# Kernel tuning notes

Hardware: AMD Instinct MI355X
Metric: run time of the kernel (lower is better)

Reference implementation:

```python
import jax, jax.numpy as jnp
import numpy as np

EMBED = 1024
HEADS = 16
HEAD_DIM = EMBED // HEADS


def setup_inputs() -> dict:
    key = jax.random.key(0)
    ks = jax.random.split(key, 8)
    N, S = 4, 2048
    values = jax.random.normal(ks[0], (N, S, EMBED), dtype=jnp.float32)
    keys = jax.random.normal(ks[1], (N, S, EMBED), dtype=jnp.float32)
    query = jax.random.normal(ks[2], (N, S, EMBED), dtype=jnp.float32)
    mask = jnp.ones((N, 1, 1, S), dtype=jnp.int32)
    sd = 1.0 / np.sqrt(HEAD_DIM)
    Wv = jax.random.uniform(ks[3], (HEAD_DIM, HEAD_DIM), jnp.float32, -sd, sd)
    Wk = jax.random.uniform(ks[4], (HEAD_DIM, HEAD_DIM), jnp.float32, -sd, sd)
    Wq = jax.random.uniform(ks[5], (HEAD_DIM, HEAD_DIM), jnp.float32, -sd, sd)
    so = 1.0 / np.sqrt(EMBED)
    Wo = jax.random.uniform(ks[6], (EMBED, EMBED), jnp.float32, -so, so)
    bo = jax.random.uniform(ks[7], (EMBED,), jnp.float32, -so, so)
    return {"values": values, "keys": keys, "query": query, "mask": mask,
            "Wv": Wv, "Wk": Wk, "Wq": Wq, "Wo": Wo, "bo": bo}


def reference(values, keys, query, mask, Wv, Wk, Wq, Wo, bo):
    N, Sq, _ = query.shape
    # split heads: (N, L, H, D)
    v = values.reshape(N, -1, HEADS, HEAD_DIM)
    k = keys.reshape(N, -1, HEADS, HEAD_DIM)
    q = query.reshape(N, Sq, HEADS, HEAD_DIM)
    # per-head linear projections (torch Linear: x @ W.T)
    v = jnp.einsum('nlhd,ed->nlhe', v, Wv)
    k = jnp.einsum('nlhd,ed->nlhe', k, Wk)
    q = jnp.einsum('nqhd,ed->nqhe', q, Wq)
    # energy: (N, H, Q, K)
    energy = jnp.einsum('nqhd,nkhd->nhqk', q, k)
    energy = jnp.where(mask == 0, jnp.float32(-1e20), energy)
    # NOTE: original scales by sqrt(embed_size), not sqrt(head_dim)
    attention = jax.nn.softmax(energy / jnp.sqrt(jnp.float32(EMBED)), axis=3)
    out = jnp.einsum('nhql,nlhd->nqhd', attention, v).reshape(N, Sq, EMBED)
    return out @ Wo.T + bo
```

## Files before the change

### kernel.cpp

```cpp
#include <hip/hip_runtime.h>
#include <hip/hip_bf16.h>

typedef __bf16 bf16x8 __attribute__((ext_vector_type(8)));
typedef __bf16 bf16x4 __attribute__((ext_vector_type(4)));
typedef __bf16 bf16x2 __attribute__((ext_vector_type(2)));
typedef float  f32x4  __attribute__((ext_vector_type(4)));
typedef float  f32x16 __attribute__((ext_vector_type(16)));
typedef unsigned int u32;
typedef u32 u32x2 __attribute__((ext_vector_type(2)));
typedef u32 u32x4 __attribute__((ext_vector_type(4)));

#define S_  2048
#define E_  1024
#define NH_ 64

__device__ __forceinline__ f32x4 mfma16(bf16x8 a, bf16x8 b, f32x4 c) {
    return __builtin_amdgcn_mfma_f32_16x16x32_bf16(a, b, c, 0, 0, 0);
}
__device__ __forceinline__ f32x16 mfma32(bf16x8 a, bf16x8 b, f32x16 c) {
    return __builtin_amdgcn_mfma_f32_32x32x16_bf16(a, b, c, 0, 0, 0);
}
__device__ __forceinline__ u32 pack2(float a, float b) {
    bf16x2 t; t[0] = (__bf16)a; t[1] = (__bf16)b;
    return __builtin_bit_cast(u32, t);
}
__device__ __forceinline__ void swap32(u32& a, u32& b) {
    asm("v_permlane32_swap_b32 %0, %1" : "+v"(a), "+v"(b));
}
__device__ __forceinline__ f32x16 zero16() {
    f32x16 z;
#pragma unroll
    for (int i = 0; i < 16; ++i) z[i] = 0.f;
    return z;
}
__device__ __forceinline__ void gload_lds16(const void* g, void* l) {
    __builtin_amdgcn_global_load_lds(
        (const __attribute__((address_space(1))) unsigned int*)g,
        (__attribute__((address_space(3))) unsigned int*)l, 16, 0, 0);
}

__global__ __launch_bounds__(256) void k_cast_wo(const float* __restrict__ Wo,
                                                 __bf16* __restrict__ Wob) {
    int i = (blockIdx.x * 256 + threadIdx.x) * 8;
    int o = i >> 10, e0 = i & 1023;
    float4 a = *(const float4*)(Wo + i);
    float4 b = *(const float4*)(Wo + i + 4);
    bf16x8 f;
    f[0] = (__bf16)a.x; f[1] = (__bf16)a.y; f[2] = (__bf16)a.z; f[3] = (__bf16)a.w;
    f[4] = (__bf16)b.x; f[5] = (__bf16)b.y; f[6] = (__bf16)b.z; f[7] = (__bf16)b.w;
    int e_swz = (e0 & ~63) | ((e0 & 63) ^ ((o & 7) << 3));
    *(bf16x8*)(Wob + (size_t)o * 1024 + e_swz) = f;
}

#define TP 72
__global__ __launch_bounds__(256) void k_proj(const float* __restrict__ vin,
                                              const float* __restrict__ kin,
                                              const float* __restrict__ qin,
                                              const float* __restrict__ Wv,
                                              const float* __restrict__ Wk,
                                              const float* __restrict__ Wq,
                                              __bf16* __restrict__ Qws,
                                              __bf16* __restrict__ Kws,
                                              __bf16* __restrict__ Vt) {
    __shared__ __align__(16) __bf16 tile[64 * TP];
    const int z = blockIdx.z;
    const float* in = (z == 0) ? vin : ((z == 1) ? kin : qin);
    const float* W  = (z == 0) ? Wv  : ((z == 1) ? Wk  : Wq);
    const float scale = (z == 2) ? 0.04508422f : 1.0f;
    const int bid  = blockIdx.x;
    const int nh   = bid >> 3;
    const int sbase = (bid & 7) << 8;
    const int n = nh >> 4, h = nh & 15;
    const int lane = threadIdx.x & 63, wid = threadIdx.x >> 6;
    const int l16 = lane & 15, g = lane >> 4;

    bf16x8 Bf[4][2];
#pragma unroll
    for (int nt = 0; nt < 4; ++nt)
#pragma unroll
        for (int ks = 0; ks < 2; ++ks) {
            const float* wp = W + (nt * 16 + l16) * 64 + ks * 32 + g * 8;
            float4 a = *(const float4*)wp;
            float4 b = *(const float4*)(wp + 4);
            bf16x8 f;
            f[0] = (__bf16)(a.x * scale); f[1] = (__bf16)(a.y * scale);
            f[2] = (__bf16)(a.z * scale); f[3] = (__bf16)(a.w * scale);
            f[4] = (__bf16)(b.x * scale); f[5] = (__bf16)(b.y * scale);
            f[6] = (__bf16)(b.z * scale); f[7] = (__bf16)(b.w * scale);
            Bf[nt][ks] = f;
        }

    for (int it = 0; it < 4; ++it) {
        const int sblk = sbase + it * 64;
        const int s = sblk + wid * 16 + l16;
        const float* ip = in + ((size_t)n * S_ + s) * E_ + h * 64 + g * 8;
        bf16x8 Af[2];
#pragma unroll
        for (int ks = 0; ks < 2; ++ks) {
            float4 a = *(const float4*)(ip + ks * 32);
            float4 b = *(const float4*)(ip + ks * 32 + 4);
            bf16x8 f;
            f[0] = (__bf16)a.x; f[1] = (__bf16)a.y; f[2] = (__bf16)a.z; f[3] = (__bf16)a.w;
            f[4] = (__bf16)b.x; f[5] = (__bf16)b.y; f[6] = (__bf16)b.z; f[7] = (__bf16)b.w;
            Af[ks] = f;
        }

        f32x4 acc[4];
#pragma unroll
        for (int nt = 0; nt < 4; ++nt) { acc[nt][0] = 0.f; acc[nt][1] = 0.f; acc[nt][2] = 0.f; acc[nt][3] = 0.f; }

        if (it > 0) __syncthreads();
        if (z == 0) {
#pragma unroll
            for (int nt = 0; nt < 4; ++nt) {
                acc[nt] = mfma16(Af[0], Bf[nt][0], acc[nt]);
                acc[nt] = mfma16(Af[1], Bf[nt][1], acc[nt]);
            }
#pragma unroll
            for (int nt = 0; nt < 4; ++nt) {
                int d = nt * 16 + l16;
                int scol = (wid * 16 + g * 4) ^ ((d & 7) << 3);
                bf16x4 o;
#pragma unroll
                for (int r = 0; r < 4; ++r) o[r] = (__bf16)acc[nt][r];
                *(bf16x4*)(tile + d * TP + scol) = o;
            }
        } else {
#pragma unroll
            for (int nt = 0; nt < 4; ++nt) {
                acc[nt] = mfma16(Bf[nt][0], Af[0], acc[nt]);
                acc[nt] = mfma16(Bf[nt][1], Af[1], acc[nt]);
            }
            const int sl = wid * 16 + l16;
            const int fk = (z == 1) ? ((sl & 7) << 3) : 0;
#pragma unroll
            for (int nt = 0; nt < 4; ++nt) {
                int e0 = (nt * 16 + g * 4) ^ fk;
                bf16x4 o;
#pragma unroll
                for (int r = 0; r < 4; ++r) o[r] = (__bf16)acc[nt][r];
                *(bf16x4*)(tile + sl * TP + e0) = o;
            }
        }
        __syncthreads();

        const int trow = threadIdx.x >> 2, tc = (threadIdx.x & 3) * 16;
        bf16x8 v0 = *(const bf16x8*)(tile + trow * TP + tc);
        bf16x8 v1 = *(const bf16x8*)(tile + trow * TP + tc + 8);
        __bf16* dst;
        if (z == 0)      dst = Vt  + ((size_t)nh * 64 + trow) * S_ + sblk + tc;
        else if (z == 1) dst = Kws + ((size_t)nh * S_ + sblk + trow) * 64 + tc;
        else             dst = Qws + ((size_t)nh * S_ + sblk + trow) * 64 + tc;
        *(bf16x8*)dst = v0;
        *(bf16x8*)(dst + 8) = v1;
    }
}

__global__ __launch_bounds__(256, 4) void k_attn(const __bf16* __restrict__ Qws,
                                                 const __bf16* __restrict__ Kws,
                                                 const __bf16* __restrict__ Vt,
                                                 const int* __restrict__ maskp,
                                                 __bf16* __restrict__ Xws) {
    __shared__ __align__(16) char lds[2][16384];
    const int tid = threadIdx.x, lane = tid & 63, wid = tid >> 6;
    const int l31 = lane & 31, hf = lane >> 5, h8 = hf * 8;
    const int v = blockIdx.x;
    const int u = v >> 3;
    const int nh = (v & 7) * 8 + (u & 7), qb = u >> 3;
    const int n = nh >> 4, hd = nh & 15;

    int az = 0;
    for (int i = tid; i < S_; i += 256) az |= (maskp[(size_t)n * S_ + i] == 0);
    const int anyzero = __syncthreads_or(az);

    const char* Kc = (const char*)(Kws + (size_t)nh * S_ * 64);
    const char* Vc = (const char*)(Vt  + (size_t)nh * 64 * S_);
    const __bf16* Qb = Qws + (size_t)nh * S_ * 64;

    const int q0 = qb * 128 + wid * 32;
    bf16x8 Qf[4];
#pragma unroll
    for (int dt = 0; dt < 4; ++dt)
        Qf[dt] = *(const bf16x8*)(Qb + (size_t)(q0 + l31) * 64 + dt * 16 + h8);

    f32x16 acc0 = zero16(), acc1 = zero16();
    float lsum = 0.f;

    auto stage = [&](int buf, int kb) {
        char* base = &lds[buf][0];
        const char* ks = Kc + (size_t)kb * 8192 + wid * 2048 + lane * 16;
        char* kd = base + wid * 2048;
        gload_lds16(ks, kd);
        gload_lds16(ks + 1024, kd + 1024);
        const int r0 = wid * 16 + (lane >> 3);
        const char* vs = Vc + (size_t)r0 * (S_ * 2) + (size_t)kb * 128 + (lane & 7) * 16;
        char* vd = base + 8192 + wid * 2048;
        gload_lds16(vs, vd);
        gload_lds16(vs + (size_t)8 * (S_ * 2), vd + 1024);
    };

    const int swz = (l31 & 7) << 4;

    stage(0, 0);
    int buf = 0;
    for (int kb = 0; kb < 32; ++kb) {
        __syncthreads();
        if (kb < 31) stage(buf ^ 1, kb + 1);
        char* base = &lds[buf][0];
        char* vbase = base + 8192;
        const int k0 = kb * 64;
#pragma unroll
        for (int kt = 0; kt < 2; ++kt) {
            bf16x8 K0 = *(const bf16x8*)(base + (kt * 32 + l31) * 128 + (((0 * 2 + hf) * 16) ^ swz));
            bf16x8 K1 = *(const bf16x8*)(base + (kt * 32 + l31) * 128 + (((1 * 2 + hf) * 16) ^ swz));
            bf16x8 K2 = *(const bf16x8*)(base + (kt * 32 + l31) * 128 + (((2 * 2 + hf) * 16) ^ swz));
            bf16x8 K3 = *(const bf16x8*)(base + (kt * 32 + l31) * 128 + (((3 * 2 + hf) * 16) ^ swz));
            __builtin_amdgcn_s_setprio(1);
            f32x16 sA = zero16();
            sA = mfma32(K0, Qf[0], sA); sA = mfma32(K1, Qf[1], sA);
            sA = mfma32(K2, Qf[2], sA); sA = mfma32(K3, Qf[3], sA);
            __builtin_amdgcn_s_setprio(0);
            if (anyzero) {
#pragma unroll
                for (int r = 0; r < 16; ++r) {
                    int kk = k0 + kt * 32 + (r & 3) + 8 * (r >> 2) + 4 * hf;
                    if (maskp[(size_t)n * S_ + kk] == 0) sA[r] = -1e30f;
                }
            }
            float p[16];
#pragma unroll
            for (int r = 0; r < 16; ++r) p[r] = __builtin_amdgcn_exp2f(sA[r]);
            lsum += ((((p[0] + p[1]) + (p[2] + p[3])) + ((p[4] + p[5]) + (p[6] + p[7])))
                  + (((p[8] + p[9]) + (p[10] + p[11])) + ((p[12] + p[13]) + (p[14] + p[15]))));
            u32 w0 = pack2(p[0],  p[1]),  w1 = pack2(p[2],  p[3]);
            u32 w2 = pack2(p[4],  p[5]),  w3 = pack2(p[6],  p[7]);
            u32 w4 = pack2(p[8],  p[9]),  w5 = pack2(p[10], p[11]);
            u32 w6 = pack2(p[12], p[13]), w7 = pack2(p[14], p[15]);
            swap32(w0, w2); swap32(w1, w3); swap32(w4, w6); swap32(w5, w7);
            u32x4 t0; t0[0] = w0; t0[1] = w1; t0[2] = w2; t0[3] = w3;
            u32x4 t1; t1[0] = w4; t1[1] = w5; t1[2] = w6; t1[3] = w7;
            bf16x8 P0 = __builtin_bit_cast(bf16x8, t0);
            bf16x8 P1 = __builtin_bit_cast(bf16x8, t1);
            bf16x8 V00 = *(const bf16x8*)(vbase + (0 * 32 + l31) * 128 + ((((kt * 2 + 0) * 2 + hf) * 16) ^ swz));
            bf16x8 V01 = *(const bf16x8*)(vbase + (0 * 32 + l31) * 128 + ((((kt * 2 + 1) * 2 + hf) * 16) ^ swz));
            bf16x8 V10 = *(const bf16x8*)(vbase + (1 * 32 + l31) * 128 + ((((kt * 2 + 0) * 2 + hf) * 16) ^ swz));
            bf16x8 V11 = *(const bf16x8*)(vbase + (1 * 32 + l31) * 128 + ((((kt * 2 + 1) * 2 + hf) * 16) ^ swz));
            __builtin_amdgcn_s_setprio(1);
            acc0 = mfma32(V00, P0, acc0); acc0 = mfma32(V01, P1, acc0);
            acc1 = mfma32(V10, P0, acc1); acc1 = mfma32(V11, P1, acc1);
            __builtin_amdgcn_s_setprio(0);
        }
        buf ^= 1;
    }

    lsum += __shfl_xor(lsum, 32);
    const float inv = 1.0f / lsum;
    const int qg = q0 + l31;
    __bf16* Ob = Xws + ((size_t)(n * S_ + qg)) * E_ + hd * 64;
    const int qsw = (qg & 7) << 3;

    auto store_half = [&](const f32x16& a, int dv) {
#pragma unroll
        for (int rr = 0; rr < 4; ++rr) {
            bf16x4 o;
#pragma unroll
            for (int j = 0; j < 4; ++j) o[j] = (__bf16)(a[rr * 4 + j] * inv);
            int dsw = ((dv * 32 + rr * 8) ^ qsw) + hf * 4;
            *(bf16x4*)(Ob + dsw) = o;
        }
    };
    store_half(acc0, 0);
    store_half(acc1, 1);
}

__global__ __launch_bounds__(256) void k_out(const __bf16* __restrict__ Xws,
                                             const __bf16* __restrict__ Wob,
                                             const float* __restrict__ bo,
                                             float* __restrict__ out) {
    __shared__ __align__(16) char Al[2][16384];
    __shared__ __align__(16) char Bl[2][16384];
    const int tid = threadIdx.x, lane = tid & 63, wid = tid >> 6;
    const int l31 = lane & 31, hf = lane >> 5;
    const int v = blockIdx.x;
    const int id2 = (v & 7) * 64 + (v >> 3);
    const int mb = id2 >> 3, ob = id2 & 7;
    const int m0 = mb * 128, o0 = ob * 128;
    const int wr = wid >> 1, wc = wid & 1;

    const char* Xb = (const char*)Xws + (size_t)m0 * 2048;
    const char* Wb = (const char*)Wob + (size_t)o0 * 2048;
    const int r = tid >> 3, cb = (tid & 7) * 16;

    auto stage = [&](int buf, int kb) {
#pragma unroll
        for (int p = 0; p < 4; ++p) {
            gload_lds16(Xb + (size_t)(p * 32 + r) * 2048 + kb * 128 + cb,
                        &Al[buf][p * 4096 + wid * 1024]);
            gload_lds16(Wb + (size_t)(p * 32 + r) * 2048 + kb * 128 + cb,
                        &Bl[buf][p * 4096 + wid * 1024]);
        }
    };

    f32x16 acc00 = zero16(), acc01 = zero16(), acc10 = zero16(), acc11 = zero16();

    const int arow0 = (wr * 64 + l31) * 128;
    const int brow0 = (wc * 64 + l31) * 128;
    const int rsw = (l31 & 7) << 4;

    stage(0, 0);
    int buf = 0;
    for (int kb = 0; kb < 16; ++kb) {
        __syncthreads();
        if (kb < 15) stage(buf ^ 1, kb + 1);
        const char* ab = &Al[buf][0];
        const char* bb = &Bl[buf][0];
#pragma unroll
        for (int ks = 0; ks < 4; ++ks) {
            const int co = (ks * 32 + hf * 16) ^ rsw;
            bf16x8 A0 = *(const bf16x8*)(ab + arow0 + co);
            bf16x8 A1 = *(const bf16x8*)(ab + arow0 + 32 * 128 + co);
            bf16x8 B0 = *(const bf16x8*)(bb + brow0 + co);
            bf16x8 B1 = *(const bf16x8*)(bb + brow0 + 32 * 128 + co);
            __builtin_amdgcn_s_setprio(1);
            acc00 = mfma32(A0, B0, acc00);
            acc01 = mfma32(A0, B1, acc01);
            acc10 = mfma32(A1, B0, acc10);
            acc11 = mfma32(A1, B1, acc11);
            __builtin_amdgcn_s_setprio(0);
        }
        buf ^= 1;
    }

    const float bias0 = bo[o0 + wc * 64 + l31];
    const float bias1 = bo[o0 + wc * 64 + 32 + l31];
#pragma unroll
    for (int sm = 0; sm < 2; ++sm) {
        const f32x16& a0 = (sm == 0) ? acc00 : acc10;
        const f32x16& a1 = (sm == 0) ? acc01 : acc11;
#pragma unroll
        for (int rr = 0; rr < 4; ++rr)
#pragma unroll
            for (int j = 0; j < 4; ++j) {
                size_t m = (size_t)m0 + wr * 64 + sm * 32 + rr * 8 + hf * 4 + j;
                out[m * E_ + o0 + wc * 64 + l31]      = a0[rr * 4 + j] + bias0;
                out[m * E_ + o0 + wc * 64 + 32 + l31] = a1[rr * 4 + j] + bias1;
            }
    }
}

extern "C" void kernel_launch(void* const* d_in, const int* in_sizes, int n_in,
                              void* d_out, int out_size, void* d_ws, size_t ws_size,
                              hipStream_t stream) {
    const float* vin  = (const float*)d_in[0];
    const float* kin  = (const float*)d_in[1];
    const float* qin  = (const float*)d_in[2];
    const int*   mask = (const int*)d_in[3];
    const float* Wv   = (const float*)d_in[4];
    const float* Wk   = (const float*)d_in[5];
    const float* Wq   = (const float*)d_in[6];
    const float* Wo   = (const float*)d_in[7];
    const float* bo   = (const float*)d_in[8];

    __bf16* Qws = (__bf16*)d_ws;
    __bf16* Kws = Qws + (size_t)NH_ * S_ * 64;
    __bf16* Vt  = Kws + (size_t)NH_ * S_ * 64;
    __bf16* Xws = Vt  + (size_t)NH_ * S_ * 64;
    __bf16* Wob = Xws + (size_t)4 * S_ * E_;
    float* out = (float*)d_out;

    hipLaunchKernelGGL(k_cast_wo, dim3(512), dim3(256), 0, stream, Wo, Wob);
    hipLaunchKernelGGL(k_proj, dim3(512, 1, 3), dim3(256), 0, stream,
                       vin, kin, qin, Wv, Wk, Wq, Qws, Kws, Vt);
    hipLaunchKernelGGL(k_attn, dim3(1024), dim3(256), 0, stream, Qws, Kws, Vt, mask, Xws);
    hipLaunchKernelGGL(k_out, dim3(512), dim3(256), 0, stream, Xws, Wob, bo, out);
}
```

Measured before the change: 143.6 us.

## Load V fragments directly from global in attention and fold Wo cast into projection

```diff
diff --git a/kernel.cpp b/kernel.cpp
--- a/kernel.cpp
+++ b/kernel.cpp
@@ -39,19 +39,6 @@
         (__attribute__((address_space(3))) unsigned int*)l, 16, 0, 0);
 }
 
-__global__ __launch_bounds__(256) void k_cast_wo(const float* __restrict__ Wo,
-                                                 __bf16* __restrict__ Wob) {
-    int i = (blockIdx.x * 256 + threadIdx.x) * 8;
-    int o = i >> 10, e0 = i & 1023;
-    float4 a = *(const float4*)(Wo + i);
-    float4 b = *(const float4*)(Wo + i + 4);
-    bf16x8 f;
-    f[0] = (__bf16)a.x; f[1] = (__bf16)a.y; f[2] = (__bf16)a.z; f[3] = (__bf16)a.w;
-    f[4] = (__bf16)b.x; f[5] = (__bf16)b.y; f[6] = (__bf16)b.z; f[7] = (__bf16)b.w;
-    int e_swz = (e0 & ~63) | ((e0 & 63) ^ ((o & 7) << 3));
-    *(bf16x8*)(Wob + (size_t)o * 1024 + e_swz) = f;
-}
-
 #define TP 72
 __global__ __launch_bounds__(256) void k_proj(const float* __restrict__ vin,
                                               const float* __restrict__ kin,
@@ -59,11 +46,25 @@
                                               const float* __restrict__ Wv,
                                               const float* __restrict__ Wk,
                                               const float* __restrict__ Wq,
+                                              const float* __restrict__ Wo,
                                               __bf16* __restrict__ Qws,
                                               __bf16* __restrict__ Kws,
-                                              __bf16* __restrict__ Vt) {
+                                              __bf16* __restrict__ Vt,
+                                              __bf16* __restrict__ Wob) {
     __shared__ __align__(16) __bf16 tile[64 * TP];
     const int z = blockIdx.z;
+    if (z == 3) {
+        int i = (blockIdx.x * 256 + threadIdx.x) * 8;
+        int o = i >> 10, e0 = i & 1023;
+        float4 a = *(const float4*)(Wo + i);
+        float4 b = *(const float4*)(Wo + i + 4);
+        bf16x8 f;
+        f[0] = (__bf16)a.x; f[1] = (__bf16)a.y; f[2] = (__bf16)a.z; f[3] = (__bf16)a.w;
+        f[4] = (__bf16)b.x; f[5] = (__bf16)b.y; f[6] = (__bf16)b.z; f[7] = (__bf16)b.w;
+        int e_swz = (e0 & ~63) | ((e0 & 63) ^ ((o & 7) << 3));
+        *(bf16x8*)(Wob + (size_t)o * 1024 + e_swz) = f;
+        return;
+    }
     const float* in = (z == 0) ? vin : ((z == 1) ? kin : qin);
     const float* W  = (z == 0) ? Wv  : ((z == 1) ? Wk  : Wq);
     const float scale = (z == 2) ? 0.04508422f : 1.0f;
@@ -119,7 +120,7 @@
 #pragma unroll
             for (int nt = 0; nt < 4; ++nt) {
                 int d = nt * 16 + l16;
-                int scol = (wid * 16 + g * 4) ^ ((d & 7) << 3);
+                int scol = wid * 16 + g * 4;
                 bf16x4 o;
 #pragma unroll
                 for (int r = 0; r < 4; ++r) o[r] = (__bf16)acc[nt][r];
@@ -161,7 +162,7 @@
                                                  const __bf16* __restrict__ Vt,
                                                  const int* __restrict__ maskp,
                                                  __bf16* __restrict__ Xws) {
-    __shared__ __align__(16) char lds[2][16384];
+    __shared__ __align__(16) char lds[2][8192];
     const int tid = threadIdx.x, lane = tid & 63, wid = tid >> 6;
     const int l31 = lane & 31, hf = lane >> 5, h8 = hf * 8;
     const int v = blockIdx.x;
@@ -174,7 +175,7 @@
     const int anyzero = __syncthreads_or(az);
 
     const char* Kc = (const char*)(Kws + (size_t)nh * S_ * 64);
-    const char* Vc = (const char*)(Vt  + (size_t)nh * 64 * S_);
+    const __bf16* Vg = Vt + (size_t)nh * 64 * S_;
     const __bf16* Qb = Qws + (size_t)nh * S_ * 64;
 
     const int q0 = qb * 128 + wid * 32;
@@ -192,25 +193,30 @@
         char* kd = base + wid * 2048;
         gload_lds16(ks, kd);
         gload_lds16(ks + 1024, kd + 1024);
-        const int r0 = wid * 16 + (lane >> 3);
-        const char* vs = Vc + (size_t)r0 * (S_ * 2) + (size_t)kb * 128 + (lane & 7) * 16;
-        char* vd = base + 8192 + wid * 2048;
-        gload_lds16(vs, vd);
-        gload_lds16(vs + (size_t)8 * (S_ * 2), vd + 1024);
     };
 
     const int swz = (l31 & 7) << 4;
+    const __bf16* Vr0 = Vg + (size_t)l31 * S_ + h8;
+    const __bf16* Vr1 = Vg + (size_t)(32 + l31) * S_ + h8;
 
     stage(0, 0);
     int buf = 0;
     for (int kb = 0; kb < 32; ++kb) {
         __syncthreads();
+        const int vc = kb * 64;
+        bf16x8 V000 = *(const bf16x8*)(Vr0 + vc);
+        bf16x8 V001 = *(const bf16x8*)(Vr1 + vc);
+        bf16x8 V010 = *(const bf16x8*)(Vr0 + vc + 16);
+        bf16x8 V011 = *(const bf16x8*)(Vr1 + vc + 16);
+        bf16x8 V100 = *(const bf16x8*)(Vr0 + vc + 32);
+        bf16x8 V101 = *(const bf16x8*)(Vr1 + vc + 32);
+        bf16x8 V110 = *(const bf16x8*)(Vr0 + vc + 48);
+        bf16x8 V111 = *(const bf16x8*)(Vr1 + vc + 48);
         if (kb < 31) stage(buf ^ 1, kb + 1);
         char* base = &lds[buf][0];
-        char* vbase = base + 8192;
         const int k0 = kb * 64;
-#pragma unroll
-        for (int kt = 0; kt < 2; ++kt) {
+
+        auto ktbody = [&](int kt, bf16x8 Vs0t0, bf16x8 Vs0t1, bf16x8 Vs1t0, bf16x8 Vs1t1) {
             bf16x8 K0 = *(const bf16x8*)(base + (kt * 32 + l31) * 128 + (((0 * 2 + hf) * 16) ^ swz));
             bf16x8 K1 = *(const bf16x8*)(base + (kt * 32 + l31) * 128 + (((1 * 2 + hf) * 16) ^ swz));
             bf16x8 K2 = *(const bf16x8*)(base + (kt * 32 + l31) * 128 + (((2 * 2 + hf) * 16) ^ swz));
@@ -241,15 +247,13 @@
             u32x4 t1; t1[0] = w4; t1[1] = w5; t1[2] = w6; t1[3] = w7;
             bf16x8 P0 = __builtin_bit_cast(bf16x8, t0);
             bf16x8 P1 = __builtin_bit_cast(bf16x8, t1);
-            bf16x8 V00 = *(const bf16x8*)(vbase + (0 * 32 + l31) * 128 + ((((kt * 2 + 0) * 2 + hf) * 16) ^ swz));
-            bf16x8 V01 = *(const bf16x8*)(vbase + (0 * 32 + l31) * 128 + ((((kt * 2 + 1) * 2 + hf) * 16) ^ swz));
-            bf16x8 V10 = *(const bf16x8*)(vbase + (1 * 32 + l31) * 128 + ((((kt * 2 + 0) * 2 + hf) * 16) ^ swz));
-            bf16x8 V11 = *(const bf16x8*)(vbase + (1 * 32 + l31) * 128 + ((((kt * 2 + 1) * 2 + hf) * 16) ^ swz));
             __builtin_amdgcn_s_setprio(1);
-            acc0 = mfma32(V00, P0, acc0); acc0 = mfma32(V01, P1, acc0);
-            acc1 = mfma32(V10, P0, acc1); acc1 = mfma32(V11, P1, acc1);
+            acc0 = mfma32(Vs0t0, P0, acc0); acc0 = mfma32(Vs1t0, P1, acc0);
+            acc1 = mfma32(Vs0t1, P0, acc1); acc1 = mfma32(Vs1t1, P1, acc1);
             __builtin_amdgcn_s_setprio(0);
-        }
+        };
+        ktbody(0, V000, V001, V010, V011);
+        ktbody(1, V100, V101, V110, V111);
         buf ^= 1;
     }
 
@@ -368,9 +372,8 @@
     __bf16* Wob = Xws + (size_t)4 * S_ * E_;
     float* out = (float*)d_out;
 
-    hipLaunchKernelGGL(k_cast_wo, dim3(512), dim3(256), 0, stream, Wo, Wob);
-    hipLaunchKernelGGL(k_proj, dim3(512, 1, 3), dim3(256), 0, stream,
-                       vin, kin, qin, Wv, Wk, Wq, Qws, Kws, Vt);
+    hipLaunchKernelGGL(k_proj, dim3(512, 1, 4), dim3(256), 0, stream,
+                       vin, kin, qin, Wv, Wk, Wq, Wo, Qws, Kws, Vt, Wob);
     hipLaunchKernelGGL(k_attn, dim3(1024), dim3(256), 0, stream, Qws, Kws, Vt, mask, Xws);
     hipLaunchKernelGGL(k_out, dim3(512), dim3(256), 0, stream, Xws, Wob, bo, out);
 }
```

Result: slower. 196.9 us (+37.1%).
